# Kernel optimization log

Measured on AMD Instinct MI355X. Metric: run time of the kernel, lower is better.

The kernel has to match this reference:

```python
import jax, jax.numpy as jnp
import numpy as np

T, B, H = 2048, 64, 1024


def setup_inputs() -> dict:
    key = jax.random.key(0)
    k1, k2, k3 = jax.random.split(key, 3)
    hidden = jax.random.normal(k1, (1, B, H), dtype=jnp.float32)
    encoder_outputs = jax.random.normal(k2, (T, B, H), dtype=jnp.float32)
    W_attn = jax.random.normal(k3, (H, H), dtype=jnp.float32) * (1.0 / np.sqrt(H))
    b_attn = jnp.zeros((H,), dtype=jnp.float32)
    return {"hidden": hidden, "encoder_outputs": encoder_outputs,
            "W_attn": W_attn, "b_attn": b_attn}


def reference(hidden, encoder_outputs, W_attn, b_attn):
    # 'general' scoring: energy_tb = hidden_b . (W @ enc_tb + b)
    proj = jnp.einsum('tbh,gh->tbg', encoder_outputs, W_attn) + b_attn  # [T,B,H]
    scores = jnp.einsum('bh,tbh->bt', hidden[0], proj)                  # [B,T]
    attn = jax.nn.softmax(scores, axis=1)
    return attn[:, None, :]  # [B,1,T]
```

## Files before the change

kernel.cpp:

```cpp
#include <hip/hip_runtime.h>
#include <math.h>

#define T_DIM 2048
#define B_DIM 64
#define H_DIM 1024
#define TC 4

typedef float f4 __attribute__((ext_vector_type(4)));

__global__ __launch_bounds__(512) void qproj_kernel(
    const float* __restrict__ hidden,
    const float* __restrict__ W,
    float* __restrict__ q) {
    const int b    = blockIdx.y;
    const int h0   = blockIdx.x * 256;
    const int wave = threadIdx.x >> 6;
    const int lane = threadIdx.x & 63;

    __shared__ float hs[H_DIM];
    __shared__ f4    part[8][64];

    for (int i = threadIdx.x; i < H_DIM; i += 512)
        hs[i] = hidden[b * H_DIM + i];
    __syncthreads();

    const int gbase = wave * 128;
    const f4* Wv = (const f4*)(W + (size_t)gbase * H_DIM + h0);
    f4 acc = {0.f, 0.f, 0.f, 0.f};
#pragma unroll 8
    for (int g = 0; g < 128; ++g) {
        const float hg = hs[gbase + g];
        const f4    wv = Wv[g * 256 + lane];
        acc += hg * wv;
    }
    part[wave][lane] = acc;
    __syncthreads();

    if (wave == 0) {
        f4 s = part[0][lane];
#pragma unroll
        for (int w = 1; w < 8; ++w) s += part[w][lane];
        ((f4*)(q + (size_t)b * H_DIM + h0))[lane] = s;
    }
}

__global__ __launch_bounds__(512) void scores_kernel(
    const float* __restrict__ enc,
    const float* __restrict__ q,
    float* __restrict__ scores_t) {
    const int wave = threadIdx.x >> 6;
    const int lane = threadIdx.x & 63;
    const int t0   = blockIdx.x * TC;
    const int b0   = blockIdx.y * 16 + wave * 2;

    f4 qf0[4], qf1[4];
    {
        const f4* qv0 = (const f4*)(q + (size_t)b0 * H_DIM);
        const f4* qv1 = (const f4*)(q + (size_t)(b0 + 1) * H_DIM);
#pragma unroll
        for (int k = 0; k < 4; ++k) {
            qf0[k] = qv0[k * 64 + lane];
            qf1[k] = qv1[k * 64 + lane];
        }
    }

#pragma unroll
    for (int tt = 0; tt < TC; ++tt) {
        const int t = t0 + tt;
        const f4* e0p = (const f4*)(enc + ((size_t)t * B_DIM + b0) * H_DIM);
        const f4* e1p = e0p + 256;

        f4 E0[4], E1[4];
#pragma unroll
        for (int k = 0; k < 4; ++k) E0[k] = e0p[k * 64 + lane];
#pragma unroll
        for (int k = 0; k < 4; ++k) E1[k] = e1p[k * 64 + lane];

        float a0 = 0.f, a1 = 0.f;
#pragma unroll
        for (int k = 0; k < 4; ++k) {
            a0 += E0[k].x * qf0[k].x + E0[k].y * qf0[k].y +
                  E0[k].z * qf0[k].z + E0[k].w * qf0[k].w;
            a1 += E1[k].x * qf1[k].x + E1[k].y * qf1[k].y +
                  E1[k].z * qf1[k].z + E1[k].w * qf1[k].w;
        }

        const bool odd = lane & 1;
        float m = odd ? a1 : a0;
        float o = odd ? a0 : a1;
        m += __shfl_xor(o, 1);
#pragma unroll
        for (int off = 2; off < 64; off <<= 1)
            m += __shfl_xor(m, off);

        if (lane < 2)
            scores_t[(size_t)t * B_DIM + b0 + lane] = m;
    }
}

__global__ __launch_bounds__(512) void softmax_kernel(
    const float* __restrict__ scores_t,
    float* __restrict__ out) {
    const int b    = blockIdx.x;
    const int tid  = threadIdx.x;
    const int wave = tid >> 6;
    const int lane = tid & 63;

    float v[4];
#pragma unroll
    for (int j = 0; j < 4; ++j)
        v[j] = scores_t[(size_t)(tid * 4 + j) * B_DIM + b];

    float m = fmaxf(fmaxf(v[0], v[1]), fmaxf(v[2], v[3]));
#pragma unroll
    for (int off = 1; off < 64; off <<= 1)
        m = fmaxf(m, __shfl_xor(m, off));

    __shared__ float redm[8], reds[8];
    if (lane == 0) redm[wave] = m;
    __syncthreads();
    m = redm[0];
#pragma unroll
    for (int w = 1; w < 8; ++w) m = fmaxf(m, redm[w]);

    float s = 0.f;
#pragma unroll
    for (int j = 0; j < 4; ++j) {
        v[j] = expf(v[j] - m);
        s += v[j];
    }
#pragma unroll
    for (int off = 1; off < 64; off <<= 1)
        s += __shfl_xor(s, off);
    if (lane == 0) reds[wave] = s;
    __syncthreads();
    s = reds[0];
#pragma unroll
    for (int w = 1; w < 8; ++w) s += reds[w];

    const float inv = 1.0f / s;
    f4 ov = {v[0] * inv, v[1] * inv, v[2] * inv, v[3] * inv};
    ((f4*)(out + (size_t)b * T_DIM))[tid] = ov;
}

extern "C" void kernel_launch(void* const* d_in, const int* in_sizes, int n_in,
                              void* d_out, int out_size, void* d_ws, size_t ws_size,
                              hipStream_t stream) {
    const float* hidden = (const float*)d_in[0];
    const float* enc    = (const float*)d_in[1];
    const float* W      = (const float*)d_in[2];

    float* out      = (float*)d_out;
    float* q        = (float*)d_ws;
    float* scores_t = (float*)d_ws + (size_t)B_DIM * H_DIM;

    qproj_kernel  <<<dim3(H_DIM / 256, B_DIM),       512, 0, stream>>>(hidden, W, q);
    scores_kernel <<<dim3(T_DIM / TC, B_DIM / 16),   512, 0, stream>>>(enc, q, scores_t);
    softmax_kernel<<<dim3(B_DIM),                    512, 0, stream>>>(scores_t, out);
}
```

Baseline: 119.6 us.

## Batch four rows per qproj block, double scores t-chunk, use nontemporal loads

The query projection kernel now handles four batch rows per block, so each W element loaded is reused across four accumulators and W is read from memory a quarter as often. The scores kernel processes eight timesteps per block with a partial unroll, and reads encoder outputs through nontemporal loads to avoid polluting cache with streamed data. These changes trade fewer blocks, and so less parallelism, for more reuse and lower launch-grid overhead.

```diff
diff --git a/kernel.cpp b/kernel.cpp
--- a/kernel.cpp
+++ b/kernel.cpp
@@ -4,7 +4,7 @@
 #define T_DIM 2048
 #define B_DIM 64
 #define H_DIM 1024
-#define TC 4
+#define TC 8
 
 typedef float f4 __attribute__((ext_vector_type(4)));
 
@@ -12,35 +12,40 @@
     const float* __restrict__ hidden,
     const float* __restrict__ W,
     float* __restrict__ q) {
-    const int b    = blockIdx.y;
+    const int b0   = blockIdx.y * 4;
     const int h0   = blockIdx.x * 256;
     const int wave = threadIdx.x >> 6;
     const int lane = threadIdx.x & 63;
 
-    __shared__ float hs[H_DIM];
-    __shared__ f4    part[8][64];
+    __shared__ float hs[4][H_DIM];
+    __shared__ f4    part[8][4][64];
 
-    for (int i = threadIdx.x; i < H_DIM; i += 512)
-        hs[i] = hidden[b * H_DIM + i];
+    for (int i = threadIdx.x; i < 4 * H_DIM; i += 512)
+        hs[i >> 10][i & 1023] = hidden[(size_t)b0 * H_DIM + i];
     __syncthreads();
 
     const int gbase = wave * 128;
     const f4* Wv = (const f4*)(W + (size_t)gbase * H_DIM + h0);
-    f4 acc = {0.f, 0.f, 0.f, 0.f};
-#pragma unroll 8
+    f4 acc0 = {0,0,0,0}, acc1 = {0,0,0,0}, acc2 = {0,0,0,0}, acc3 = {0,0,0,0};
+#pragma unroll 4
     for (int g = 0; g < 128; ++g) {
-        const float hg = hs[gbase + g];
-        const f4    wv = Wv[g * 256 + lane];
-        acc += hg * wv;
+        const f4 wv = Wv[g * 256 + lane];
+        acc0 += hs[0][gbase + g] * wv;
+        acc1 += hs[1][gbase + g] * wv;
+        acc2 += hs[2][gbase + g] * wv;
+        acc3 += hs[3][gbase + g] * wv;
     }
-    part[wave][lane] = acc;
+    part[wave][0][lane] = acc0;
+    part[wave][1][lane] = acc1;
+    part[wave][2][lane] = acc2;
+    part[wave][3][lane] = acc3;
     __syncthreads();
 
-    if (wave == 0) {
-        f4 s = part[0][lane];
+    if (wave < 4) {
+        f4 s = part[0][wave][lane];
 #pragma unroll
-        for (int w = 1; w < 8; ++w) s += part[w][lane];
-        ((f4*)(q + (size_t)b * H_DIM + h0))[lane] = s;
+        for (int w = 1; w < 8; ++w) s += part[w][wave][lane];
+        ((f4*)(q + (size_t)(b0 + wave) * H_DIM + h0))[lane] = s;
     }
 }
 
@@ -64,7 +69,7 @@
         }
     }
 
-#pragma unroll
+#pragma unroll 2
     for (int tt = 0; tt < TC; ++tt) {
         const int t = t0 + tt;
         const f4* e0p = (const f4*)(enc + ((size_t)t * B_DIM + b0) * H_DIM);
@@ -72,9 +77,11 @@
 
         f4 E0[4], E1[4];
 #pragma unroll
-        for (int k = 0; k < 4; ++k) E0[k] = e0p[k * 64 + lane];
+        for (int k = 0; k < 4; ++k)
+            E0[k] = __builtin_nontemporal_load(&e0p[k * 64 + lane]);
 #pragma unroll
-        for (int k = 0; k < 4; ++k) E1[k] = e1p[k * 64 + lane];
+        for (int k = 0; k < 4; ++k)
+            E1[k] = __builtin_nontemporal_load(&e1p[k * 64 + lane]);
 
         float a0 = 0.f, a1 = 0.f;
 #pragma unroll
@@ -154,7 +161,7 @@
     float* q        = (float*)d_ws;
     float* scores_t = (float*)d_ws + (size_t)B_DIM * H_DIM;
 
-    qproj_kernel  <<<dim3(H_DIM / 256, B_DIM),       512, 0, stream>>>(hidden, W, q);
-    scores_kernel <<<dim3(T_DIM / TC, B_DIM / 16),   512, 0, stream>>>(enc, q, scores_t);
-    softmax_kernel<<<dim3(B_DIM),                    512, 0, stream>>>(scores_t, out);
+    qproj_kernel  <<<dim3(H_DIM / 256, B_DIM / 4), 512, 0, stream>>>(hidden, W, q);
+    scores_kernel <<<dim3(T_DIM / TC, B_DIM / 16), 512, 0, stream>>>(enc, q, scores_t);
+    softmax_kernel<<<dim3(B_DIM),                  512, 0, stream>>>(scores_t, out);
 }
```

Result: faster. 100.5 us (-15.9%).
